# Performance work log

Hardware: AMD Instinct MI355X
Metric: run time of the kernel (lower is better)

## Reference

```python
import jax, jax.numpy as jnp
import numpy as np

NUM_BINS = 256
BN_EPS = 1e-5


def setup_inputs() -> dict:
    key = jax.random.key(0)
    ks = jax.random.split(key, 16)
    B, C, H, W = 16, 64, 256, 256
    x = jax.random.uniform(ks[0], (B, C, H, W), dtype=jnp.float32) * 255.0
    return {
        "x": x,
        "conv1_w": jax.random.normal(ks[1], (C, C), dtype=jnp.float32) * 0.05,
        "conv1_b": jax.random.normal(ks[2], (C,), dtype=jnp.float32) * 0.05,
        "bn1_gamma": jax.random.uniform(ks[3], (C,), dtype=jnp.float32) + 0.5,
        "bn1_beta": jax.random.normal(ks[4], (C,), dtype=jnp.float32) * 0.05,
        "bn1_mean": jax.random.normal(ks[5], (C,), dtype=jnp.float32) * 0.05,
        "bn1_var": jax.random.uniform(ks[6], (C,), dtype=jnp.float32) + 0.5,
        "conv2_w": jax.random.normal(ks[7], (1, C), dtype=jnp.float32) * 0.05,
        "conv2_b": jax.random.normal(ks[8], (1,), dtype=jnp.float32) * 0.05,
        "bn2_gamma": jax.random.uniform(ks[9], (1,), dtype=jnp.float32) + 0.5,
        "bn2_beta": jax.random.normal(ks[10], (1,), dtype=jnp.float32) * 0.05,
        "bn2_mean": jax.random.normal(ks[11], (1,), dtype=jnp.float32) * 0.05,
        "bn2_var": jax.random.uniform(ks[12], (1,), dtype=jnp.float32) + 0.5,
    }


def _histc_argmax(x):
    # Replicates torch.histc(v, bins=NUM_BINS, min=0, max=255) per (b, c)
    # followed by argmax over bins. Out-of-range values are ignored by histc.
    B, C, H, W = x.shape
    flat = x.reshape(B * C, H * W)
    in_range = (flat >= 0.0) & (flat <= 255.0)
    # histc bin index: floor((v - min) * bins / (max - min)); v == max -> last bin
    idx = jnp.clip((flat * (NUM_BINS / 255.0)).astype(jnp.int32), 0, NUM_BINS - 1)
    rows = jnp.arange(B * C)[:, None]
    hist = jnp.zeros((B * C, NUM_BINS), dtype=jnp.float32).at[rows, idx].add(
        in_range.astype(jnp.float32)
    )
    return hist.argmax(axis=-1).reshape(B, C)  # [B, C] dominant bin indices


def _bn(a, gamma, beta, mean, var):
    inv = gamma * jax.lax.rsqrt(var + BN_EPS)
    return a * inv[None, :, None, None] + (beta - mean * inv)[None, :, None, None]


def reference(x, conv1_w, conv1_b, bn1_gamma, bn1_beta, bn1_mean, bn1_var,
              conv2_w, conv2_b, bn2_gamma, bn2_beta, bn2_mean, bn2_var):
    bin_size = 256 // NUM_BINS  # == 1 for default num_bins
    dominant = _histc_argmax(x)  # [B, C]
    # per-pixel bin index: torch's x.float() // bin_size then .long()
    pixel_bins = jnp.floor(x / bin_size).astype(jnp.int32)  # [B, C, H, W]
    att = (pixel_bins != dominant[:, :, None, None]).astype(x.dtype)
    # conv1 (1x1) -> bn1 -> relu
    a = jnp.einsum('bchw,oc->bohw', att, conv1_w) + conv1_b[None, :, None, None]
    a = jax.nn.relu(_bn(a, bn1_gamma, bn1_beta, bn1_mean, bn1_var))
    # conv2 (1x1, C->1) -> bn2 -> sigmoid
    a = jnp.einsum('bchw,oc->bohw', a, conv2_w) + conv2_b[None, :, None, None]
    a = jax.nn.sigmoid(_bn(a, bn2_gamma, bn2_beta, bn2_mean, bn2_var))
    return x * a
```

## Files before the change

### kernel.cpp

```cpp
#include <hip/hip_runtime.h>
#include <stdint.h>

#define CCH 64
#define HWPIX 65536
#define NBINS 256


__global__ __launch_bounds__(64) void precomp_kernel(
    const float* __restrict__ w1, const float* __restrict__ b1,
    const float* __restrict__ g1, const float* __restrict__ be1,
    const float* __restrict__ m1, const float* __restrict__ v1,
    const float* __restrict__ w2, const float* __restrict__ b2,
    const float* __restrict__ g2, const float* __restrict__ be2,
    const float* __restrict__ m2, const float* __restrict__ v2,
    float* __restrict__ ws)
{
    int o = threadIdx.x;
    float inv1 = g1[o] * rsqrtf(v1[o] + 1e-5f);
    float S = 0.f;
    for (int c = 0; c < CCH; ++c) S += w1[o * CCH + c];
    float beta1p = be1[o] - m1[o] * inv1;
    float base_pre = (S + b1[o]) * inv1 + beta1p;
    for (int c = 0; c < CCH; ++c) ws[1024 + o * CCH + c] = w1[o * CCH + c] * inv1;
    ws[5120 + o] = base_pre;
    float w2o = w2[o];
    ws[5184 + o] = w2o;
    float t = fmaxf(base_pre, 0.f) * w2o;
    #pragma unroll
    for (int off = 32; off > 0; off >>= 1) t += __shfl_down(t, off, 64);
    if (o == 0) {
        float inv2 = g2[0] * rsqrtf(v2[0] + 1e-5f);
        float beta2p = be2[0] - m2[0] * inv2;
        float z = (t + b2[0]) * inv2 + beta2p;
        ws[5248] = inv2;
        ws[5249] = beta2p;
        ws[5250] = b2[0];
        ws[5251] = 1.f / (1.f + expf(-z));
    }
}

__global__ __launch_bounds__(256) void hist_kernel(
    const float* __restrict__ x, int* __restrict__ dom)
{
    __shared__ unsigned h[4][NBINS];
    __shared__ unsigned long long red[NBINS];
    int tid = threadIdx.x;
    const float4* xp = (const float4*)(x + (size_t)blockIdx.x * HWPIX);

    for (int i = tid; i < 4 * NBINS; i += 256) ((unsigned*)h)[i] = 0;
    __syncthreads();

    unsigned* hmine = h[tid >> 6];
    const float scale = 256.0f / 255.0f;
    #pragma unroll 4
    for (int t = 0; t < HWPIX / 4 / 256; ++t) {
        float4 v = xp[t * 256 + tid];
        float vv[4] = {v.x, v.y, v.z, v.w};
        #pragma unroll
        for (int j = 0; j < 4; ++j) {
            float f = vv[j];
            if (f >= 0.f && f <= 255.f) {
                int bi = (int)(f * scale);
                bi = bi > NBINS - 1 ? NBINS - 1 : bi;
                atomicAdd(&hmine[bi], 1u);
            }
        }
    }
    __syncthreads();

    unsigned cnt = h[0][tid] + h[1][tid] + h[2][tid] + h[3][tid];
    red[tid] = ((unsigned long long)cnt << 32) | (unsigned)(NBINS - 1 - tid);
    __syncthreads();
    #pragma unroll
    for (int s = 128; s > 0; s >>= 1) {
        if (tid < s) {
            unsigned long long a = red[tid], b = red[tid + s];
            red[tid] = a > b ? a : b;
        }
        __syncthreads();
    }
    if (tid == 0) dom[blockIdx.x] = (NBINS - 1) - (int)(red[0] & 0xffffffffu);
}

__global__ __launch_bounds__(256) void main_kernel(
    const float* __restrict__ x, const float* __restrict__ ws,
    const int* __restrict__ dom, float* __restrict__ out)
{
    __shared__ float WcolT[CCH * CCH];
    __shared__ float bp_s[CCH];
    __shared__ float w2_s[CCH];
    __shared__ int   dom_s[CCH];
    __shared__ float sc[4];

    int tid = threadIdx.x;
    int b = blockIdx.x >> 8;
    int hw = ((blockIdx.x & 255) << 8) | tid;

    for (int i = tid; i < CCH * CCH; i += 256) WcolT[i] = ws[1024 + i];
    if (tid < CCH) {
        bp_s[tid]  = ws[5120 + tid];
        w2_s[tid]  = ws[5184 + tid];
        dom_s[tid] = dom[b * CCH + tid];
    }
    if (tid < 4) sc[tid] = ws[5248 + tid];
    __syncthreads();

    const float* xb = x + ((size_t)b << 22);
    float vx[CCH];
    #pragma unroll
    for (int c = 0; c < CCH; ++c) vx[c] = xb[((size_t)c << 16) + hw];

    unsigned long long m = 0ull;
    #pragma unroll
    for (int c = 0; c < CCH; ++c)
        m |= (unsigned long long)((int)floorf(vx[c]) == dom_s[c]) << c;

    float s;
    if (m == 0ull) {
        s = sc[3];
    } else {
        float t = 0.f;
        for (int o = 0; o < CCH; ++o) {
            float acc = bp_s[o];
            unsigned long long mm = m;
            const float* row = &WcolT[o << 6];
            while (mm) {
                int c = __builtin_ctzll(mm);
                mm &= mm - 1;
                acc -= row[c];
            }
            t += fmaxf(acc, 0.f) * w2_s[o];
        }
        float z = (t + sc[2]) * sc[0] + sc[1];
        s = 1.f / (1.f + expf(-z));
    }

    float* ob = out + ((size_t)b << 22);
    #pragma unroll
    for (int c = 0; c < CCH; ++c) ob[((size_t)c << 16) + hw] = vx[c] * s;
}

extern "C" void kernel_launch(void* const* d_in, const int* in_sizes, int n_in,
                              void* d_out, int out_size, void* d_ws, size_t ws_size,
                              hipStream_t stream) {
    const float* x   = (const float*)d_in[0];
    const float* w1  = (const float*)d_in[1];
    const float* b1  = (const float*)d_in[2];
    const float* g1  = (const float*)d_in[3];
    const float* be1 = (const float*)d_in[4];
    const float* m1  = (const float*)d_in[5];
    const float* v1  = (const float*)d_in[6];
    const float* w2  = (const float*)d_in[7];
    const float* b2  = (const float*)d_in[8];
    const float* g2  = (const float*)d_in[9];
    const float* be2 = (const float*)d_in[10];
    const float* m2  = (const float*)d_in[11];
    const float* v2  = (const float*)d_in[12];

    float* ws  = (float*)d_ws;
    int*   dom = (int*)d_ws;
    float* outp = (float*)d_out;

    int B = in_sizes[0] / (CCH * HWPIX);

    precomp_kernel<<<1, 64, 0, stream>>>(w1, b1, g1, be1, m1, v1,
                                         w2, b2, g2, be2, m2, v2, ws);
    hist_kernel<<<B * CCH, 256, 0, stream>>>(x, dom);
    main_kernel<<<B * (HWPIX / 256), 256, 0, stream>>>(x, ws, dom, outp);
}
```

Measured before the change: 190.0 us.

## Precompute single-hit sigmoid table, widen histogram privatization, stream stores

```diff
diff --git a/kernel.cpp b/kernel.cpp
--- a/kernel.cpp
+++ b/kernel.cpp
@@ -37,20 +37,31 @@
         ws[5250] = b2[0];
         ws[5251] = 1.f / (1.f + expf(-z));
     }
+    __syncthreads();
+    {
+        int c = o;
+        float t1 = 0.f;
+        for (int oo = 0; oo < CCH; ++oo) {
+            float acc = ws[5120 + oo] - ws[1024 + oo * CCH + c];
+            t1 += fmaxf(acc, 0.f) * ws[5184 + oo];
+        }
+        float z = (t1 + ws[5250]) * ws[5248] + ws[5249];
+        ws[5312 + c] = 1.f / (1.f + expf(-z));
+    }
 }
 
 __global__ __launch_bounds__(256) void hist_kernel(
     const float* __restrict__ x, int* __restrict__ dom)
 {
-    __shared__ unsigned h[4][NBINS];
+    __shared__ unsigned h[16][NBINS + 1];
     __shared__ unsigned long long red[NBINS];
     int tid = threadIdx.x;
     const float4* xp = (const float4*)(x + (size_t)blockIdx.x * HWPIX);
 
-    for (int i = tid; i < 4 * NBINS; i += 256) ((unsigned*)h)[i] = 0;
+    for (int i = tid; i < 16 * (NBINS + 1); i += 256) ((unsigned*)h)[i] = 0;
     __syncthreads();
 
-    unsigned* hmine = h[tid >> 6];
+    unsigned* hmine = h[tid >> 4];
     const float scale = 256.0f / 255.0f;
     #pragma unroll 4
     for (int t = 0; t < HWPIX / 4 / 256; ++t) {
@@ -68,7 +79,9 @@
     }
     __syncthreads();
 
-    unsigned cnt = h[0][tid] + h[1][tid] + h[2][tid] + h[3][tid];
+    unsigned cnt = 0;
+    #pragma unroll
+    for (int k = 0; k < 16; ++k) cnt += h[k][tid];
     red[tid] = ((unsigned long long)cnt << 32) | (unsigned)(NBINS - 1 - tid);
     __syncthreads();
     #pragma unroll
@@ -86,23 +99,19 @@
     const float* __restrict__ x, const float* __restrict__ ws,
     const int* __restrict__ dom, float* __restrict__ out)
 {
-    __shared__ float WcolT[CCH * CCH];
-    __shared__ float bp_s[CCH];
-    __shared__ float w2_s[CCH];
-    __shared__ int   dom_s[CCH];
-    __shared__ float sc[4];
+    __shared__ float df[CCH];
+    __shared__ float s1_s[CCH];
+    __shared__ float sc4[4];
 
     int tid = threadIdx.x;
     int b = blockIdx.x >> 8;
     int hw = ((blockIdx.x & 255) << 8) | tid;
 
-    for (int i = tid; i < CCH * CCH; i += 256) WcolT[i] = ws[1024 + i];
     if (tid < CCH) {
-        bp_s[tid]  = ws[5120 + tid];
-        w2_s[tid]  = ws[5184 + tid];
-        dom_s[tid] = dom[b * CCH + tid];
+        df[tid]   = (float)dom[b * CCH + tid];
+        s1_s[tid] = ws[5312 + tid];
     }
-    if (tid < 4) sc[tid] = ws[5248 + tid];
+    if (tid < 4) sc4[tid] = ws[5248 + tid];
     __syncthreads();
 
     const float* xb = x + ((size_t)b << 22);
@@ -112,32 +121,37 @@
 
     unsigned long long m = 0ull;
     #pragma unroll
-    for (int c = 0; c < CCH; ++c)
-        m |= (unsigned long long)((int)floorf(vx[c]) == dom_s[c]) << c;
+    for (int c = 0; c < CCH; ++c) {
+        float d = df[c];
+        m |= (unsigned long long)(vx[c] >= d && vx[c] < d + 1.0f) << c;
+    }
 
     float s;
     if (m == 0ull) {
-        s = sc[3];
+        s = sc4[3];
+    } else if ((m & (m - 1)) == 0ull) {
+        s = s1_s[__builtin_ctzll(m)];
     } else {
         float t = 0.f;
         for (int o = 0; o < CCH; ++o) {
-            float acc = bp_s[o];
+            float acc = ws[5120 + o];
             unsigned long long mm = m;
-            const float* row = &WcolT[o << 6];
+            const float* row = ws + 1024 + (o << 6);
             while (mm) {
                 int c = __builtin_ctzll(mm);
                 mm &= mm - 1;
                 acc -= row[c];
             }
-            t += fmaxf(acc, 0.f) * w2_s[o];
+            t += fmaxf(acc, 0.f) * ws[5184 + o];
         }
-        float z = (t + sc[2]) * sc[0] + sc[1];
+        float z = (t + sc4[2]) * sc4[0] + sc4[1];
         s = 1.f / (1.f + expf(-z));
     }
 
     float* ob = out + ((size_t)b << 22);
     #pragma unroll
-    for (int c = 0; c < CCH; ++c) ob[((size_t)c << 16) + hw] = vx[c] * s;
+    for (int c = 0; c < CCH; ++c)
+        __builtin_nontemporal_store(vx[c] * s, &ob[((size_t)c << 16) + hw]);
 }
 
 extern "C" void kernel_launch(void* const* d_in, const int* in_sizes, int n_in,
```

Result: no change. 193.1 us (+1.6%).
